# Kernel tuning notes

Measured on AMD Instinct MI355X. Metric: run time of the kernel, lower is better.

## Reference

```python
import jax, jax.numpy as jnp
import numpy as np

B, T, C, H = 2, 2048, 1024, 16
HS = C // H  # head size = 64


def _rope_cos_sin(t, hs):
    # theta_i = 1/10000^(2(i-1)/hs) for i in [1, hs/2]
    pos = jnp.arange(t, dtype=jnp.float32)[:, None]          # [T,1]
    i = jnp.arange(1, hs // 2 + 1, dtype=jnp.float32)[None]  # [1,hs/2]
    theta = 1.0 / 10000.0 ** (2.0 * (i - 1.0) / hs)
    ang = pos * theta                                        # [T,hs/2]
    return jnp.cos(ang), jnp.sin(ang)


def _apply_rope(u, cos, sin):
    # u: [B,H,T,HS]; complex multiply on consecutive pairs
    u2 = u.reshape(*u.shape[:-1], HS // 2, 2)
    x0, x1 = u2[..., 0], u2[..., 1]
    c = cos[None, None]  # [1,1,T,hs/2]
    s = sin[None, None]
    r0 = x0 * c - x1 * s
    r1 = x0 * s + x1 * c
    return jnp.stack([r0, r1], axis=-1).reshape(u.shape)


def setup_inputs() -> dict:
    key = jax.random.key(0)
    ks = jax.random.split(key, 5)
    return {
        "x": jax.random.normal(ks[0], (B, T, C), dtype=jnp.float32),
        "W_qkv": jax.random.normal(ks[1], (C, 3 * C), dtype=jnp.float32) * 0.02,
        "b_qkv": jax.random.normal(ks[2], (3 * C,), dtype=jnp.float32) * 0.02,
        "W_proj": jax.random.normal(ks[3], (C, C), dtype=jnp.float32) * 0.02,
        "b_proj": jax.random.normal(ks[4], (C,), dtype=jnp.float32) * 0.02,
    }


def reference(x, W_qkv, b_qkv, W_proj, b_proj):
    b, t, c = x.shape
    qkv = x @ W_qkv + b_qkv                                   # [B,T,3C]
    qkv = qkv.reshape(b, t, H, 3 * HS).transpose(0, 2, 1, 3)  # [B,H,T,3*HS]
    q, k, v = jnp.split(qkv, 3, axis=-1)                      # each [B,H,T,HS]

    cos, sin = _rope_cos_sin(t, HS)
    q = _apply_rope(q, cos, sin)
    k = _apply_rope(k, cos, sin)

    att = jnp.einsum("bhqd,bhkd->bhqk", q, k) / jnp.sqrt(jnp.float32(HS))
    causal = jnp.tril(jnp.ones((t, t), dtype=bool))[None, None]
    att = jnp.where(causal, att, jnp.float32(-1e9))
    att = jax.nn.softmax(att, axis=-1)
    y = jnp.einsum("bhqk,bhkd->bhqd", att, v)                 # [B,H,T,HS]
    y = y.transpose(0, 2, 1, 3).reshape(b, t, c)
    return y @ W_proj + b_proj
```

## Files before the change

### kernel.cpp

```cpp
#include <hip/hip_runtime.h>

typedef unsigned short u16;
typedef unsigned int u32;
typedef __bf16 bf16x8 __attribute__((ext_vector_type(8)));
typedef float f32x4 __attribute__((ext_vector_type(4)));
typedef u16 u16x4 __attribute__((ext_vector_type(4)));
typedef u16 u16x8 __attribute__((ext_vector_type(8)));

__device__ __forceinline__ u16 f2bf(float f) {
  u32 u = __builtin_bit_cast(u32, f);
  u += 0x7fffu + ((u >> 16) & 1u);
  return (u16)(u >> 16);
}

__device__ __forceinline__ u32 pk2(float a, float b) {
  u32 ua = __builtin_bit_cast(u32, a) + 0x8000u;
  u32 ub = __builtin_bit_cast(u32, b) + 0x8000u;
  return __builtin_amdgcn_perm(ub, ua, 0x07060302);
}

__device__ __forceinline__ void gld16(const void* g, void* l) {
  __builtin_amdgcn_global_load_lds(
      (const __attribute__((address_space(1))) void*)g,
      (__attribute__((address_space(3))) void*)l, 16, 0, 0);
}

__global__ __launch_bounds__(256) void k_prep(
    const float* __restrict__ x, u16* __restrict__ xb,
    const float* __restrict__ Wqkv, u16* __restrict__ Wqkvt,
    const float* __restrict__ Wproj, u16* __restrict__ Wpt,
    float2* __restrict__ rope) {
  __shared__ float tile[32][33];
  const int tid = threadIdx.x;
  int bx = blockIdx.x;
  if (bx < 4096) {
    int i = (bx * 256 + tid) * 4;
    float4 v = *(const float4*)(x + i);
    u16x4 o = { f2bf(v.x), f2bf(v.y), f2bf(v.z), f2bf(v.w) };
    *(u16x4*)(xb + i) = o;
    return;
  }
  bx -= 4096;
  const float* src; u16* dst; int R, Cc, bxx, byy;
  if (bx < 3072) {
    src = Wqkv; dst = Wqkvt; R = 1024; Cc = 3072; bxx = bx % 96; byy = bx / 96;
  } else if (bx < 4096) {
    int b = bx - 3072;
    src = Wproj; dst = Wpt; R = 1024; Cc = 1024; bxx = b % 32; byy = b / 32;
  } else {
    int i = (bx - 4096) * 256 + tid;
    int t = i >> 5, d = i & 31;
    float theta = expf(-(float)d * 0.28782313662425575f);
    float ang = (float)t * theta;
    rope[i] = make_float2(cosf(ang), sinf(ang));
    return;
  }
  int xx = tid & 31, yy = tid >> 5;
  int c0 = bxx * 32, r0 = byy * 32;
  for (int i = 0; i < 4; ++i)
    tile[yy + 8 * i][xx] = src[(size_t)(r0 + yy + 8 * i) * Cc + c0 + xx];
  __syncthreads();
  for (int i = 0; i < 4; ++i)
    dst[(size_t)(c0 + yy + 8 * i) * R + r0 + xx] = f2bf(tile[xx][yy + 8 * i]);
}

__global__ __launch_bounds__(256, 4) void k_qkv(
    const u16* __restrict__ Xb,
    const u16* __restrict__ Wt,
    const float* __restrict__ bias,
    const float2* __restrict__ rope,
    u16* __restrict__ Qg,
    u16* __restrict__ Kg,
    u16* __restrict__ Vt) {
  __shared__ alignas(16) u16 smem[18432];
  u16* As = smem;
  u16* Bs = smem + 8192;
  const int tid = threadIdx.x;
  const int lane = tid & 63, w = tid >> 6;
  const int quad = lane >> 4, l15 = lane & 15;
  const int m0 = blockIdx.y * 128, n0 = blockIdx.x * 128;
  const int wm = (w & 1) * 64, wn = (w >> 1) * 64;
  const int srow = lane >> 3, sj = lane & 7;
  const int sw = (sj ^ srow) * 8;
  const f32x4 vzero = {0.f, 0.f, 0.f, 0.f};

  f32x4 acc[4][4];
  for (int i = 0; i < 4; ++i)
    for (int j = 0; j < 4; ++j) acc[i][j] = vzero;

  for (int kt = 0; kt < 1024; kt += 64) {
    __syncthreads();
    for (int i = 0; i < 4; ++i) {
      int row = w * 32 + i * 8;
      gld16(Xb + (size_t)(m0 + row + srow) * 1024 + kt + sw, &As[row * 64]);
      gld16(Wt + (size_t)(n0 + row + srow) * 1024 + kt + sw, &Bs[row * 64]);
    }
    __syncthreads();
    for (int ks = 0; ks < 2; ++ks) {
      const int cc = ((ks * 4 + quad) ^ (l15 & 7)) * 8;
      bf16x8 a[4], b[4];
      for (int mt = 0; mt < 4; ++mt)
        a[mt] = *(const bf16x8*)&As[(wm + mt * 16 + l15) * 64 + cc];
      for (int nt = 0; nt < 4; ++nt)
        b[nt] = *(const bf16x8*)&Bs[(wn + nt * 16 + l15) * 64 + cc];
      for (int nt = 0; nt < 4; ++nt)
        for (int mt = 0; mt < 4; ++mt)
          acc[nt][mt] = __builtin_amdgcn_mfma_f32_16x16x32_bf16(
              b[nt], a[mt], acc[nt][mt], 0, 0, 0);
    }
  }
  __syncthreads();

  const int half = w >> 1;
  const int nh = n0 + half * 64;
  const int region = (nh % 192) >> 6;
  u16* Eh = smem + half * 9216;
  if (region < 2) {
    for (int nt = 0; nt < 4; ++nt) {
      float4 bv4 = *(const float4*)&bias[nh + nt * 16 + quad * 4];
      for (int mt = 0; mt < 4; ++mt) {
        int m_l = wm + mt * 16 + l15;
        int t = (m0 + m_l) & 2047;
        float4 cs = *(const float4*)&rope[t * 32 + nt * 8 + quad * 2];
        float v0 = acc[nt][mt][0] + bv4.x;
        float v1 = acc[nt][mt][1] + bv4.y;
        float v2 = acc[nt][mt][2] + bv4.z;
        float v3 = acc[nt][mt][3] + bv4.w;
        float r0 = fmaf(-v1, cs.y, v0 * cs.x);
        float r1 = fmaf( v0, cs.y, v1 * cs.x);
        float r2 = fmaf(-v3, cs.w, v2 * cs.z);
        float r3 = fmaf( v2, cs.w, v3 * cs.z);
        uint2 pv; pv.x = pk2(r0, r1); pv.y = pk2(r2, r3);
        *(uint2*)&Eh[m_l * 72 + nt * 16 + quad * 4] = pv;
      }
    }
  } else {
    for (int nt = 0; nt < 4; ++nt) {
      float4 bv4 = *(const float4*)&bias[nh + nt * 16 + quad * 4];
      for (int mt = 0; mt < 4; ++mt) {
        int m_l = wm + mt * 16 + l15;
        int cb = nt * 16 + quad * 4;
        Eh[(cb + 0) * 136 + m_l] = f2bf(acc[nt][mt][0] + bv4.x);
        Eh[(cb + 1) * 136 + m_l] = f2bf(acc[nt][mt][1] + bv4.y);
        Eh[(cb + 2) * 136 + m_l] = f2bf(acc[nt][mt][2] + bv4.z);
        Eh[(cb + 3) * 136 + m_l] = f2bf(acc[nt][mt][3] + bv4.w);
      }
    }
  }
  __syncthreads();

  const int bb = m0 >> 11, t0 = m0 & 2047;
  for (int hf = 0; hf < 2; ++hf) {
    const int nhf = n0 + hf * 64;
    const int hh = nhf / 192;
    const int reg = (nhf % 192) >> 6;
    const u16* Ef = smem + hf * 9216;
    if (reg < 2) {
      u16* dst = (reg == 0 ? Qg : Kg) +
                 ((size_t)(bb * 16 + hh) * 2048 + t0) * 64;
      int chunk = tid & 7, row0 = tid >> 3;
      for (int p = 0; p < 4; ++p) {
        int row = row0 + p * 32;
        u16x8 val = *(const u16x8*)&Ef[row * 72 + chunk * 8];
        *(u16x8*)(dst + (size_t)row * 64 + chunk * 8) = val;
      }
    } else {
      u16* dstv = Vt + (size_t)(bb * 16 + hh) * 64 * 2048 + t0;
      int mch = tid & 15, c0r = tid >> 4;
      for (int p = 0; p < 4; ++p) {
        int c = c0r + p * 16;
        u16x8 val = *(const u16x8*)&Ef[c * 136 + mch * 8];
        *(u16x8*)(dstv + (size_t)c * 2048 + mch * 8) = val;
      }
    }
  }
}

__global__ __launch_bounds__(512, 4) void k_attn(
    const u16* __restrict__ Qg, const u16* __restrict__ Kg,
    const u16* __restrict__ Vt, u16* __restrict__ Og) {
  __shared__ alignas(16) u16 Ks[2][64 * 64];
  __shared__ alignas(16) u16 Vs[2][64 * 64];
  __shared__ alignas(16) u16 Ps[128 * 72];
  const int tid = threadIdx.x, lane = tid & 63, w = tid >> 6;
  const int quad = lane >> 4, l15 = lane & 15;
  const int bh = blockIdx.y;
  int tmp = (blockIdx.x + bh) & 15;
  const int qt = (bh & 16) ? (15 - tmp) : tmp;
  const int q0 = qt * 128;
  const u16* Qh = Qg + (size_t)bh * 2048 * 64;
  const u16* Kh = Kg + (size_t)bh * 2048 * 64;
  const u16* Vh = Vt + (size_t)bh * 64 * 2048;
  const f32x4 vzero = {0.f, 0.f, 0.f, 0.f};
  const float SCL = 0.125f * 1.4426950408889634f;
  const int myrow = w * 16;

  bf16x8 aq[2];
  {
    const u16* qp = Qh + (size_t)(q0 + myrow + l15) * 64 + quad * 8;
    aq[0] = *(const bf16x8*)(qp);
    aq[1] = *(const bf16x8*)(qp + 32);
  }

  const int r8 = lane >> 3, j8 = lane & 7;
  const int sw_c = (j8 ^ r8) * 8;

  float lsum = 0.f;
  f32x4 O[4];
  for (int nt = 0; nt < 4; ++nt) O[nt] = vzero;

  const int nk = 2 * qt + 2;
  gld16(Kh + (size_t)(w * 8 + r8) * 64 + sw_c, &Ks[0][w * 8 * 64]);
  gld16(Vh + (size_t)(w * 8 + r8) * 2048 + sw_c, &Vs[0][w * 8 * 64]);

  for (int kb = 0; kb < nk; ++kb) {
    const int k0 = kb * 64;
    const int cur = kb & 1;
    __syncthreads();
    if (kb + 1 < nk) {
      const int k1 = k0 + 64;
      gld16(Kh + (size_t)(k1 + w * 8 + r8) * 64 + sw_c, &Ks[cur ^ 1][w * 8 * 64]);
      gld16(Vh + (size_t)(w * 8 + r8) * 2048 + k1 + sw_c, &Vs[cur ^ 1][w * 8 * 64]);
    }
    if (k0 > q0 + myrow + 15) continue;

    f32x4 st[4];
    for (int nt = 0; nt < 4; ++nt) st[nt] = vzero;
    for (int ks = 0; ks < 2; ++ks) {
      bf16x8 ak[4];
      for (int nt = 0; nt < 4; ++nt)
        ak[nt] = *(const bf16x8*)&Ks[cur][(nt * 16 + l15) * 64 +
                                         ((ks * 4 + quad) ^ (l15 & 7)) * 8];
      for (int nt = 0; nt < 4; ++nt)
        st[nt] = __builtin_amdgcn_mfma_f32_16x16x32_bf16(ak[nt], aq[ks], st[nt], 0, 0, 0);
    }

    if (k0 + 63 <= q0 + myrow) {
      for (int nt = 0; nt < 4; ++nt) {
        float p0 = __builtin_amdgcn_exp2f(st[nt][0] * SCL);
        float p1 = __builtin_amdgcn_exp2f(st[nt][1] * SCL);
        float p2 = __builtin_amdgcn_exp2f(st[nt][2] * SCL);
        float p3 = __builtin_amdgcn_exp2f(st[nt][3] * SCL);
        lsum += (p0 + p1) + (p2 + p3);
        uint2 pv; pv.x = pk2(p0, p1); pv.y = pk2(p2, p3);
        *(uint2*)&Ps[(myrow + l15) * 72 + nt * 16 + quad * 4] = pv;
      }
    } else {
      const int tq = q0 + myrow + l15;
      const int kbase = k0 + quad * 4;
      for (int nt = 0; nt < 4; ++nt) {
        float p[4];
        for (int r = 0; r < 4; ++r) {
          float pv = __builtin_amdgcn_exp2f(st[nt][r] * SCL);
          p[r] = (kbase + nt * 16 + r <= tq) ? pv : 0.f;
          lsum += p[r];
        }
        uint2 pv; pv.x = pk2(p[0], p[1]); pv.y = pk2(p[2], p[3]);
        *(uint2*)&Ps[(myrow + l15) * 72 + nt * 16 + quad * 4] = pv;
      }
    }

    for (int ks = 0; ks < 2; ++ks) {
      bf16x8 a = *(const bf16x8*)&Ps[(myrow + l15) * 72 + ks * 32 + quad * 8];
      bf16x8 bv[4];
      for (int nt = 0; nt < 4; ++nt)
        bv[nt] = *(const bf16x8*)&Vs[cur][(nt * 16 + l15) * 64 +
                                         ((ks * 4 + quad) ^ (l15 & 7)) * 8];
      for (int nt = 0; nt < 4; ++nt)
        O[nt] = __builtin_amdgcn_mfma_f32_16x16x32_bf16(a, bv[nt], O[nt], 0, 0, 0);
    }
  }

  lsum += __shfl_xor(lsum, 16, 64);
  lsum += __shfl_xor(lsum, 32, 64);
  float inv[4];
  for (int r = 0; r < 4; ++r)
    inv[r] = 1.0f / __shfl(lsum, quad * 4 + r, 16);

  for (int nt = 0; nt < 4; ++nt)
    for (int r = 0; r < 4; ++r)
      Ps[(myrow + quad * 4 + r) * 72 + nt * 16 + l15] = f2bf(O[nt][r] * inv[r]);
  __syncthreads();
  const int bb = bh >> 4, h = bh & 15;
  u16* dst = Og + ((size_t)bb * 2048 + q0) * 1024 + h * 64;
  int chunk = tid & 7, row0 = tid >> 3;
  for (int p = 0; p < 2; ++p) {
    int row = row0 + p * 64;
    u16x8 val = *(const u16x8*)&Ps[row * 72 + chunk * 8];
    *(u16x8*)(dst + (size_t)row * 1024 + chunk * 8) = val;
  }
}

__global__ __launch_bounds__(256, 4) void k_proj(
    const u16* __restrict__ Ag,
    const u16* __restrict__ Wt,
    const float* __restrict__ bias,
    float* __restrict__ out) {
  __shared__ alignas(16) u16 As[64 * 64];
  __shared__ alignas(16) u16 Bs[128 * 64];
  const int tid = threadIdx.x;
  const int lane = tid & 63, w = tid >> 6;
  const int quad = lane >> 4, l15 = lane & 15;
  const int m0 = blockIdx.y * 64, n0 = blockIdx.x * 128;
  const int wm = (w & 1) * 32, wn = (w >> 1) * 64;
  const int srow = lane >> 3, sj = lane & 7;
  const int sw = (sj ^ srow) * 8;
  const f32x4 vzero = {0.f, 0.f, 0.f, 0.f};

  f32x4 acc[2][4];
  for (int i = 0; i < 2; ++i)
    for (int j = 0; j < 4; ++j) acc[i][j] = vzero;

  for (int kt = 0; kt < 1024; kt += 64) {
    __syncthreads();
    for (int i = 0; i < 2; ++i) {
      int row = w * 16 + i * 8;
      gld16(Ag + (size_t)(m0 + row + srow) * 1024 + kt + sw, &As[row * 64]);
    }
    for (int i = 0; i < 4; ++i) {
      int row = w * 32 + i * 8;
      gld16(Wt + (size_t)(n0 + row + srow) * 1024 + kt + sw, &Bs[row * 64]);
    }
    __syncthreads();
    for (int ks = 0; ks < 2; ++ks) {
      const int cc = ((ks * 4 + quad) ^ (l15 & 7)) * 8;
      bf16x8 a[2], b[4];
      for (int mt = 0; mt < 2; ++mt)
        a[mt] = *(const bf16x8*)&As[(wm + mt * 16 + l15) * 64 + cc];
      for (int nt = 0; nt < 4; ++nt)
        b[nt] = *(const bf16x8*)&Bs[(wn + nt * 16 + l15) * 64 + cc];
      for (int mt = 0; mt < 2; ++mt)
        for (int nt = 0; nt < 4; ++nt)
          acc[mt][nt] = __builtin_amdgcn_mfma_f32_16x16x32_bf16(
              a[mt], b[nt], acc[mt][nt], 0, 0, 0);
    }
  }

  for (int nt = 0; nt < 4; ++nt) {
    int n = n0 + wn + nt * 16 + l15;
    float bv = bias[n];
    for (int mt = 0; mt < 2; ++mt)
      for (int r = 0; r < 4; ++r) {
        int m = m0 + wm + mt * 16 + quad * 4 + r;
        out[(size_t)m * 1024 + n] = acc[mt][nt][r] + bv;
      }
  }
}

extern "C" void kernel_launch(void* const* d_in, const int* in_sizes, int n_in,
                              void* d_out, int out_size, void* d_ws, size_t ws_size,
                              hipStream_t stream) {
  (void)in_sizes; (void)n_in; (void)out_size; (void)ws_size;
  const float* x     = (const float*)d_in[0];
  const float* Wqkv  = (const float*)d_in[1];
  const float* bqkv  = (const float*)d_in[2];
  const float* Wproj = (const float*)d_in[3];
  const float* bproj = (const float*)d_in[4];
  float* out = (float*)d_out;

  char* ws = (char*)d_ws;
  size_t off = 0;
  u16* Xb    = (u16*)(ws + off); off += (size_t)4096 * 1024 * 2;
  u16* Wqkvt = (u16*)(ws + off); off += (size_t)3072 * 1024 * 2;
  u16* Wpt   = (u16*)(ws + off); off += (size_t)1024 * 1024 * 2;
  u16* Qg    = (u16*)(ws + off); off += (size_t)2 * 16 * 2048 * 64 * 2;
  u16* Kg    = (u16*)(ws + off); off += (size_t)2 * 16 * 2048 * 64 * 2;
  u16* Vt    = (u16*)(ws + off); off += (size_t)2 * 16 * 64 * 2048 * 2;
  u16* Att   = (u16*)(ws + off); off += (size_t)4096 * 1024 * 2;
  float2* rope = (float2*)(ws + off); off += (size_t)2048 * 32 * sizeof(float2);

  k_prep<<<8448, 256, 0, stream>>>(x, Xb, Wqkv, Wqkvt, Wproj, Wpt, rope);
  k_qkv<<<dim3(24, 32), 256, 0, stream>>>(Xb, Wqkvt, bqkv, rope, Qg, Kg, Vt);
  k_attn<<<dim3(16, 32), 512, 0, stream>>>(Qg, Kg, Vt, Att);
  k_proj<<<dim3(8, 64), 256, 0, stream>>>(Att, Wpt, bproj, out);
}
```

Baseline: 174.6 us.

## Pair causal 64-row query tiles per attention block for load balance

The attention kernel moves from 512-thread blocks owning one 128-row query tile to 256-thread blocks that each process two 64-row tiles, qt and 31-qt. Every block therefore does the same total amount of causal work. The first K/V block for the second tile is prefetched during the last iteration of the first tile, which keeps the double-buffer pipeline running across tiles. The aim is to remove the tail imbalance and idle warps caused by causal masking. In exchange, each block has fewer warps to hide latency and runs more sequential iterations.

```diff
diff --git a/kernel.cpp b/kernel.cpp
--- a/kernel.cpp
+++ b/kernel.cpp
@@ -176,118 +176,126 @@
   }
 }
 
-__global__ __launch_bounds__(512, 4) void k_attn(
+__global__ __launch_bounds__(256, 4) void k_attn(
     const u16* __restrict__ Qg, const u16* __restrict__ Kg,
     const u16* __restrict__ Vt, u16* __restrict__ Og) {
   __shared__ alignas(16) u16 Ks[2][64 * 64];
   __shared__ alignas(16) u16 Vs[2][64 * 64];
-  __shared__ alignas(16) u16 Ps[128 * 72];
+  __shared__ alignas(16) u16 Ps[64 * 72];
   const int tid = threadIdx.x, lane = tid & 63, w = tid >> 6;
   const int quad = lane >> 4, l15 = lane & 15;
   const int bh = blockIdx.y;
-  int tmp = (blockIdx.x + bh) & 15;
-  const int qt = (bh & 16) ? (15 - tmp) : tmp;
-  const int q0 = qt * 128;
   const u16* Qh = Qg + (size_t)bh * 2048 * 64;
   const u16* Kh = Kg + (size_t)bh * 2048 * 64;
   const u16* Vh = Vt + (size_t)bh * 64 * 2048;
   const f32x4 vzero = {0.f, 0.f, 0.f, 0.f};
   const float SCL = 0.125f * 1.4426950408889634f;
   const int myrow = w * 16;
-
-  bf16x8 aq[2];
-  {
-    const u16* qp = Qh + (size_t)(q0 + myrow + l15) * 64 + quad * 8;
-    aq[0] = *(const bf16x8*)(qp);
-    aq[1] = *(const bf16x8*)(qp + 32);
-  }
+  const int bb = bh >> 4, h = bh & 15;
 
   const int r8 = lane >> 3, j8 = lane & 7;
   const int sw_c = (j8 ^ r8) * 8;
 
-  float lsum = 0.f;
-  f32x4 O[4];
-  for (int nt = 0; nt < 4; ++nt) O[nt] = vzero;
-
-  const int nk = 2 * qt + 2;
-  gld16(Kh + (size_t)(w * 8 + r8) * 64 + sw_c, &Ks[0][w * 8 * 64]);
-  gld16(Vh + (size_t)(w * 8 + r8) * 2048 + sw_c, &Vs[0][w * 8 * 64]);
-
-  for (int kb = 0; kb < nk; ++kb) {
-    const int k0 = kb * 64;
-    const int cur = kb & 1;
-    __syncthreads();
-    if (kb + 1 < nk) {
-      const int k1 = k0 + 64;
-      gld16(Kh + (size_t)(k1 + w * 8 + r8) * 64 + sw_c, &Ks[cur ^ 1][w * 8 * 64]);
-      gld16(Vh + (size_t)(w * 8 + r8) * 2048 + k1 + sw_c, &Vs[cur ^ 1][w * 8 * 64]);
-    }
-    if (k0 > q0 + myrow + 15) continue;
-
-    f32x4 st[4];
-    for (int nt = 0; nt < 4; ++nt) st[nt] = vzero;
-    for (int ks = 0; ks < 2; ++ks) {
-      bf16x8 ak[4];
-      for (int nt = 0; nt < 4; ++nt)
-        ak[nt] = *(const bf16x8*)&Ks[cur][(nt * 16 + l15) * 64 +
-                                         ((ks * 4 + quad) ^ (l15 & 7)) * 8];
-      for (int nt = 0; nt < 4; ++nt)
-        st[nt] = __builtin_amdgcn_mfma_f32_16x16x32_bf16(ak[nt], aq[ks], st[nt], 0, 0, 0);
-    }
-
-    if (k0 + 63 <= q0 + myrow) {
-      for (int nt = 0; nt < 4; ++nt) {
-        float p0 = __builtin_amdgcn_exp2f(st[nt][0] * SCL);
-        float p1 = __builtin_amdgcn_exp2f(st[nt][1] * SCL);
-        float p2 = __builtin_amdgcn_exp2f(st[nt][2] * SCL);
-        float p3 = __builtin_amdgcn_exp2f(st[nt][3] * SCL);
-        lsum += (p0 + p1) + (p2 + p3);
-        uint2 pv; pv.x = pk2(p0, p1); pv.y = pk2(p2, p3);
-        *(uint2*)&Ps[(myrow + l15) * 72 + nt * 16 + quad * 4] = pv;
-      }
-    } else {
-      const int tq = q0 + myrow + l15;
-      const int kbase = k0 + quad * 4;
-      for (int nt = 0; nt < 4; ++nt) {
-        float p[4];
-        for (int r = 0; r < 4; ++r) {
-          float pv = __builtin_amdgcn_exp2f(st[nt][r] * SCL);
-          p[r] = (kbase + nt * 16 + r <= tq) ? pv : 0.f;
-          lsum += p[r];
+  for (int i = 0; i < 2; ++i) {
+    int row = w * 16 + i * 8;
+    gld16(Kh + (size_t)(row + r8) * 64 + sw_c, &Ks[0][row * 64]);
+    gld16(Vh + (size_t)(row + r8) * 2048 + sw_c, &Vs[0][row * 64]);
+  }
+
+  int buf = 0;
+  const int tiles[2] = {(int)blockIdx.x, 31 - (int)blockIdx.x};
+  for (int ti = 0; ti < 2; ++ti) {
+    const int qt = tiles[ti];
+    const int q0 = qt * 64;
+    bf16x8 aq[2];
+    {
+      const u16* qp = Qh + (size_t)(q0 + myrow + l15) * 64 + quad * 8;
+      aq[0] = *(const bf16x8*)(qp);
+      aq[1] = *(const bf16x8*)(qp + 32);
+    }
+    float lsum = 0.f;
+    f32x4 O[4];
+    for (int nt = 0; nt < 4; ++nt) O[nt] = vzero;
+
+    const int nk = qt + 1;
+    for (int kb = 0; kb < nk; ++kb) {
+      const int k0 = kb * 64;
+      __syncthreads();
+      int nxt = (kb + 1 < nk) ? (k0 + 64) : (ti == 0 ? 0 : -1);
+      if (nxt >= 0) {
+        for (int i = 0; i < 2; ++i) {
+          int row = w * 16 + i * 8;
+          gld16(Kh + (size_t)(nxt + row + r8) * 64 + sw_c, &Ks[buf ^ 1][row * 64]);
+          gld16(Vh + (size_t)(row + r8) * 2048 + nxt + sw_c, &Vs[buf ^ 1][row * 64]);
         }
-        uint2 pv; pv.x = pk2(p[0], p[1]); pv.y = pk2(p[2], p[3]);
-        *(uint2*)&Ps[(myrow + l15) * 72 + nt * 16 + quad * 4] = pv;
-      }
-    }
-
-    for (int ks = 0; ks < 2; ++ks) {
-      bf16x8 a = *(const bf16x8*)&Ps[(myrow + l15) * 72 + ks * 32 + quad * 8];
-      bf16x8 bv[4];
-      for (int nt = 0; nt < 4; ++nt)
-        bv[nt] = *(const bf16x8*)&Vs[cur][(nt * 16 + l15) * 64 +
-                                         ((ks * 4 + quad) ^ (l15 & 7)) * 8];
-      for (int nt = 0; nt < 4; ++nt)
-        O[nt] = __builtin_amdgcn_mfma_f32_16x16x32_bf16(a, bv[nt], O[nt], 0, 0, 0);
-    }
-  }
-
-  lsum += __shfl_xor(lsum, 16, 64);
-  lsum += __shfl_xor(lsum, 32, 64);
-  float inv[4];
-  for (int r = 0; r < 4; ++r)
-    inv[r] = 1.0f / __shfl(lsum, quad * 4 + r, 16);
-
-  for (int nt = 0; nt < 4; ++nt)
+      }
+
+      f32x4 st[4];
+      for (int nt = 0; nt < 4; ++nt) st[nt] = vzero;
+      for (int ks = 0; ks < 2; ++ks) {
+        bf16x8 ak[4];
+        for (int nt = 0; nt < 4; ++nt)
+          ak[nt] = *(const bf16x8*)&Ks[buf][(nt * 16 + l15) * 64 +
+                                           ((ks * 4 + quad) ^ (l15 & 7)) * 8];
+        for (int nt = 0; nt < 4; ++nt)
+          st[nt] = __builtin_amdgcn_mfma_f32_16x16x32_bf16(ak[nt], aq[ks], st[nt], 0, 0, 0);
+      }
+
+      if (kb < qt) {
+        for (int nt = 0; nt < 4; ++nt) {
+          float p0 = __builtin_amdgcn_exp2f(st[nt][0] * SCL);
+          float p1 = __builtin_amdgcn_exp2f(st[nt][1] * SCL);
+          float p2 = __builtin_amdgcn_exp2f(st[nt][2] * SCL);
+          float p3 = __builtin_amdgcn_exp2f(st[nt][3] * SCL);
+          lsum += (p0 + p1) + (p2 + p3);
+          uint2 pv; pv.x = pk2(p0, p1); pv.y = pk2(p2, p3);
+          *(uint2*)&Ps[(myrow + l15) * 72 + nt * 16 + quad * 4] = pv;
+        }
+      } else {
+        const int tq = q0 + myrow + l15;
+        const int kbase = k0 + quad * 4;
+        for (int nt = 0; nt < 4; ++nt) {
+          float p[4];
+          for (int r = 0; r < 4; ++r) {
+            float pv = __builtin_amdgcn_exp2f(st[nt][r] * SCL);
+            p[r] = (kbase + nt * 16 + r <= tq) ? pv : 0.f;
+            lsum += p[r];
+          }
+          uint2 pv; pv.x = pk2(p[0], p[1]); pv.y = pk2(p[2], p[3]);
+          *(uint2*)&Ps[(myrow + l15) * 72 + nt * 16 + quad * 4] = pv;
+        }
+      }
+
+      for (int ks = 0; ks < 2; ++ks) {
+        bf16x8 a = *(const bf16x8*)&Ps[(myrow + l15) * 72 + ks * 32 + quad * 8];
+        bf16x8 bv[4];
+        for (int nt = 0; nt < 4; ++nt)
+          bv[nt] = *(const bf16x8*)&Vs[buf][(nt * 16 + l15) * 64 +
+                                           ((ks * 4 + quad) ^ (l15 & 7)) * 8];
+        for (int nt = 0; nt < 4; ++nt)
+          O[nt] = __builtin_amdgcn_mfma_f32_16x16x32_bf16(a, bv[nt], O[nt], 0, 0, 0);
+      }
+      buf ^= 1;
+    }
+
+    float ls = lsum;
+    ls += __shfl_xor(ls, 16, 64);
+    ls += __shfl_xor(ls, 32, 64);
+    float inv[4];
     for (int r = 0; r < 4; ++r)
-      Ps[(myrow + quad * 4 + r) * 72 + nt * 16 + l15] = f2bf(O[nt][r] * inv[r]);
-  __syncthreads();
-  const int bb = bh >> 4, h = bh & 15;
-  u16* dst = Og + ((size_t)bb * 2048 + q0) * 1024 + h * 64;
-  int chunk = tid & 7, row0 = tid >> 3;
-  for (int p = 0; p < 2; ++p) {
-    int row = row0 + p * 64;
-    u16x8 val = *(const u16x8*)&Ps[row * 72 + chunk * 8];
-    *(u16x8*)(dst + (size_t)row * 1024 + chunk * 8) = val;
+      inv[r] = 1.0f / __shfl(ls, quad * 4 + r, 16);
+
+    for (int nt = 0; nt < 4; ++nt)
+      for (int r = 0; r < 4; ++r)
+        Ps[(myrow + quad * 4 + r) * 72 + nt * 16 + l15] = f2bf(O[nt][r] * inv[r]);
+    __syncthreads();
+    u16* dst = Og + ((size_t)bb * 2048 + q0) * 1024 + h * 64;
+    int chunk = tid & 7, row0 = tid >> 3;
+    for (int p = 0; p < 2; ++p) {
+      int row = row0 + p * 32;
+      u16x8 val = *(const u16x8*)&Ps[row * 72 + chunk * 8];
+      *(u16x8*)(dst + (size_t)row * 1024 + chunk * 8) = val;
+    }
   }
 }
 
@@ -371,6 +379,6 @@
 
   k_prep<<<8448, 256, 0, stream>>>(x, Xb, Wqkv, Wqkvt, Wproj, Wpt, rope);
   k_qkv<<<dim3(24, 32), 256, 0, stream>>>(Xb, Wqkvt, bqkv, rope, Qg, Kg, Vt);
-  k_attn<<<dim3(16, 32), 512, 0, stream>>>(Qg, Kg, Vt, Att);
+  k_attn<<<dim3(16, 32), 256, 0, stream>>>(Qg, Kg, Vt, Att);
   k_proj<<<dim3(8, 64), 256, 0, stream>>>(Att, Wpt, bproj, out);
 }
```

Measured after the change: 178.4 us. 2.2% more time.
